# Performance work log

Measured on AMD Instinct MI355X. Metric: run time of the kernel, lower is better.

Reference implementation:

```python
import jax, jax.numpy as jnp
import numpy as np

L, B, E = 512, 4, 256
SCALE = 0.05  # keep sigmoid in a non-saturated range


def setup_inputs() -> dict:
    key = jax.random.key(0)
    ks = jax.random.split(key, 6)
    return {
        "emb": jax.random.normal(ks[0], (L, B, E), dtype=jnp.float32),
        "w1": jax.random.normal(ks[1], (E, E), dtype=jnp.float32) * SCALE,
        "w2": jax.random.normal(ks[2], (E, E), dtype=jnp.float32) * SCALE,
        "w3": jax.random.normal(ks[3], (E, E), dtype=jnp.float32) * SCALE,
        "b3": jax.random.normal(ks[4], (E,), dtype=jnp.float32) * SCALE,
        "w0": jax.random.normal(ks[5], (E,), dtype=jnp.float32) * SCALE,
    }


def reference(emb, w1, w2, w3, b3, w0):
    # emb: (L, B, E). torch Linear computes x @ W.T (+ b).
    Lq = emb.shape[0]
    u = jnp.einsum('lbe,fe->lbf', emb, w1)                      # w1(x_i), per key i
    q = jnp.einsum('lbe,fe->lbf', emb, w2)                      # w2(x_t), per query t
    c = jnp.einsum('lbe,fe->lbf', jnp.cumsum(emb, axis=0), w3) + b3  # w3(cumsum up to t)
    # gate[t, i, b, e] = sigmoid(u[i] + q[t] + c[t]); additive score via w0
    gate = jax.nn.sigmoid(u[None, :, :, :] + (q + c)[:, None, :, :])  # (L, L, B, E)
    scores = jnp.einsum('tibe,e->tib', gate, w0)                # (L, L, B)
    causal = jnp.tril(jnp.ones((Lq, Lq), dtype=emb.dtype))      # i <= t
    scores = scores * causal[:, :, None]
    # m_a[t] = sum_{i<=t} a_i * x_i
    return jnp.einsum('tib,ibe->tbe', scores, emb)              # (L, B, E)
```

## Files before the change

### kernel.cpp

```cpp
#include <hip/hip_runtime.h>
#include <hip/hip_bf16.h>

#define L_  512
#define B_  4
#define E_  256
#define TT  16
#define TI  64

typedef unsigned short u16;
#define NLOG2E (-1.44269504f)

__device__ __forceinline__ float bflo(unsigned u) { return __uint_as_float(u << 16); }
__device__ __forceinline__ float bfhi(unsigned u) { return __uint_as_float(u & 0xffff0000u); }

__device__ __forceinline__ unsigned pack_bf2(float x, float y) {
  __hip_bfloat162 h = __float22bfloat162_rn(make_float2(x, y));
  return *reinterpret_cast<unsigned*>(&h);
}

__device__ __forceinline__ float sigs(float xs) {
  float e = __builtin_amdgcn_exp2f(xs);
  return __builtin_amdgcn_rcpf(1.0f + e);
}

__global__ __launch_bounds__(256) void prescan_k(
    const float* __restrict__ emb, float* __restrict__ CE, float* __restrict__ out0) {
  const int bc = blockIdx.x;
  const int cg = threadIdx.x & 1;
  const int rk = threadIdx.x >> 1;
  const int col = bc * 8 + cg * 4;
  __shared__ float4 s_p[128][2];
  float4 part = {0.f, 0.f, 0.f, 0.f};
  for (int l = rk * 4; l < rk * 4 + 4; ++l) {
    float4 v = *(const float4*)(emb + (size_t)l * 1024 + col);
    part.x += v.x; part.y += v.y; part.z += v.z; part.w += v.w;
  }
  s_p[rk][cg] = part;
  __syncthreads();
  float4 run = {0.f, 0.f, 0.f, 0.f};
  for (int k = 0; k < rk; ++k) {
    float4 p = s_p[k][cg];
    run.x += p.x; run.y += p.y; run.z += p.z; run.w += p.w;
  }
  for (int l = rk * 4; l < rk * 4 + 4; ++l) {
    size_t o = (size_t)l * 1024 + col;
    float4 v = *(const float4*)(emb + o);
    run.x += v.x; run.y += v.y; run.z += v.z; run.w += v.w;
    *(float4*)(CE + o) = run;
  }
  const float4 z = {0.f, 0.f, 0.f, 0.f};
  float* op = out0 + ((size_t)bc * 256 + threadIdx.x) * 16;
#pragma unroll
  for (int j = 0; j < 4; ++j) *(float4*)(op + j * 4) = z;
}

__global__ __launch_bounds__(256) void gemm2_k(
    const float* __restrict__ emb, const float* __restrict__ CE,
    const float* __restrict__ w1, const float* __restrict__ w2, const float* __restrict__ w3,
    const float* __restrict__ b3, float* __restrict__ U, float* __restrict__ QC) {
  __shared__ float As[64 * 32], Ws[64 * 32];
  const int tid = threadIdx.x, tx = tid & 15, ty = tid >> 4;
  const int z = blockIdx.x;
  const bool isU = z < 128;
  const int y = isU ? z : z - 128;
  const int r0 = (y >> 2) * 64, f0 = (y & 3) * 64;
  const int nk = isU ? 8 : 16;
  float acc[4][4] = {};
  for (int kb = 0; kb < nk; ++kb) {
    const float* A = isU ? emb : (kb < 8 ? emb : CE);
    const float* W = isU ? w1 : (kb < 8 ? w2 : w3);
    const int kk = (kb & 7) * 32;
    for (int j = 0; j < 2; ++j) {
      int idx = j * 256 + tid;
      int r = idx >> 3, g = idx & 7;
      int gs = g ^ ((r >> 2) & 7);
      *(float4*)(As + r * 32 + gs * 4) = *(const float4*)(A + (size_t)(r0 + r) * E_ + kk + g * 4);
      *(float4*)(Ws + r * 32 + gs * 4) = *(const float4*)(W + (size_t)(f0 + r) * E_ + kk + g * 4);
    }
    __syncthreads();
#pragma unroll
    for (int g = 0; g < 8; ++g) {
      float4 a[4], w[4];
#pragma unroll
      for (int i = 0; i < 4; ++i) {
        int r = ty * 4 + i;
        a[i] = *(const float4*)(As + r * 32 + (g ^ ((r >> 2) & 7)) * 4);
        int f = tx * 4 + i;
        w[i] = *(const float4*)(Ws + f * 32 + (g ^ ((f >> 2) & 7)) * 4);
      }
#pragma unroll
      for (int i = 0; i < 4; ++i)
#pragma unroll
        for (int j = 0; j < 4; ++j)
          acc[i][j] += a[i].x * w[j].x + a[i].y * w[j].y + a[i].z * w[j].z + a[i].w * w[j].w;
    }
    __syncthreads();
  }
  if (isU) {
#pragma unroll
    for (int i = 0; i < 4; ++i) {
      float4 v = make_float4(acc[i][0] * NLOG2E, acc[i][1] * NLOG2E,
                             acc[i][2] * NLOG2E, acc[i][3] * NLOG2E);
      *(float4*)(U + (size_t)(r0 + ty * 4 + i) * E_ + f0 + tx * 4) = v;
    }
  } else {
    float4 bb = *(const float4*)(b3 + f0 + tx * 4);
#pragma unroll
    for (int i = 0; i < 4; ++i) {
      float4 v = make_float4(NLOG2E * (acc[i][0] + bb.x), NLOG2E * (acc[i][1] + bb.y),
                             NLOG2E * (acc[i][2] + bb.z), NLOG2E * (acc[i][3] + bb.w));
      *(float4*)(QC + (size_t)(r0 + ty * 4 + i) * E_ + f0 + tx * 4) = v;
    }
  }
}

__global__ __launch_bounds__(512, 8) void attn_main_k(
    const float* __restrict__ emb, const float* __restrict__ U,
    const float* __restrict__ QC, const float* __restrict__ w0g,
    float* __restrict__ out) {
  const int t0 = blockIdx.x * TT, i0 = blockIdx.y * TI, b = blockIdx.z;
  if (i0 > t0) return;

  __shared__ u16 tile[TI * 264];
  __shared__ float s_s[TT][TI];
  const int tid = threadIdx.x, wave = tid >> 6, lane = tid & 63;

  {
    const float* src = U + ((size_t)i0 * B_ + b) * E_ + lane * 4;
#pragma unroll
    for (int c = 0; c < 8; ++c) {
      int r = c * 8 + wave;
      float4 v = *(const float4*)(src + (size_t)r * (B_ * E_));
      *(uint2*)(tile + r * 264 + lane * 4) =
          make_uint2(pack_bf2(v.x, v.y), pack_bf2(v.z, v.w));
    }
  }
  __syncthreads();

  const int tA = t0 + wave * 2, tB = tA + 1;
  {
    int rA = __builtin_amdgcn_readfirstlane(tA * B_ + b);
    int rB = __builtin_amdgcn_readfirstlane(tB * B_ + b);
    const float* qA = QC + (size_t)rA * E_;
    const float* qB = QC + (size_t)rB * E_;
    const u16* urow = tile + lane * 264;
    float a0 = 0.f, a1 = 0.f, a2 = 0.f, a3 = 0.f;
    float c0 = 0.f, c1 = 0.f, c2 = 0.f, c3 = 0.f;
#pragma unroll 4
    for (int g = 0; g < 32; ++g) {
      uint4 raw = *(const uint4*)(urow + g * 8);
      float4 z0 = *(const float4*)(w0g + g * 8);
      float4 z1 = *(const float4*)(w0g + g * 8 + 4);
      float4 qa0 = *(const float4*)(qA + g * 8);
      float4 qa1 = *(const float4*)(qA + g * 8 + 4);
      float4 qb0 = *(const float4*)(qB + g * 8);
      float4 qb1 = *(const float4*)(qB + g * 8 + 4);
      float u0 = bflo(raw.x), u1 = bfhi(raw.x), u2 = bflo(raw.y), u3 = bfhi(raw.y);
      float u4 = bflo(raw.z), u5 = bfhi(raw.z), u6 = bflo(raw.w), u7 = bfhi(raw.w);
      a0 += z0.x * sigs(u0 + qa0.x); a1 += z0.y * sigs(u1 + qa0.y);
      a2 += z0.z * sigs(u2 + qa0.z); a3 += z0.w * sigs(u3 + qa0.w);
      a0 += z1.x * sigs(u4 + qa1.x); a1 += z1.y * sigs(u5 + qa1.y);
      a2 += z1.z * sigs(u6 + qa1.z); a3 += z1.w * sigs(u7 + qa1.w);
      c0 += z0.x * sigs(u0 + qb0.x); c1 += z0.y * sigs(u1 + qb0.y);
      c2 += z0.z * sigs(u2 + qb0.z); c3 += z0.w * sigs(u3 + qb0.w);
      c0 += z1.x * sigs(u4 + qb1.x); c1 += z1.y * sigs(u5 + qb1.y);
      c2 += z1.z * sigs(u6 + qb1.z); c3 += z1.w * sigs(u7 + qb1.w);
    }
    float sA = (a0 + a1) + (a2 + a3), sB = (c0 + c1) + (c2 + c3);
    int i = i0 + lane;
    s_s[wave * 2][lane]     = (i <= tA) ? sA : 0.f;
    s_s[wave * 2 + 1][lane] = (i <= tB) ? sB : 0.f;
  }
  __syncthreads();

  {
    const float* embp = emb + ((size_t)i0 * B_ + b) * E_ + lane * 4;
    const float* sAv = s_s[wave * 2];
    const float* sBv = s_s[wave * 2 + 1];
    int nI = min(TI, tB - i0 + 1);
    nI = (nI + 3) & ~3;
    float4 o0 = {0.f, 0.f, 0.f, 0.f}, o1 = {0.f, 0.f, 0.f, 0.f};
    for (int i = 0; i < nI; i += 4) {
#pragma unroll
      for (int k2 = 0; k2 < 4; ++k2) {
        float4 r = *(const float4*)(embp + (size_t)(i + k2) * (B_ * E_));
        float sa = sAv[i + k2], sb = sBv[i + k2];
        o0.x += sa * r.x; o0.y += sa * r.y; o0.z += sa * r.z; o0.w += sa * r.w;
        o1.x += sb * r.x; o1.y += sb * r.y; o1.z += sb * r.z; o1.w += sb * r.w;
      }
    }
    float* opA = out + ((size_t)tA * B_ + b) * E_ + lane * 4;
    float* opB = out + ((size_t)tB * B_ + b) * E_ + lane * 4;
    atomicAdd(opA + 0, o0.x); atomicAdd(opA + 1, o0.y);
    atomicAdd(opA + 2, o0.z); atomicAdd(opA + 3, o0.w);
    atomicAdd(opB + 0, o1.x); atomicAdd(opB + 1, o1.y);
    atomicAdd(opB + 2, o1.z); atomicAdd(opB + 3, o1.w);
  }
}

extern "C" void kernel_launch(void* const* d_in, const int* in_sizes, int n_in,
                              void* d_out, int out_size, void* d_ws, size_t ws_size,
                              hipStream_t stream) {
  const float* emb = (const float*)d_in[0];
  const float* w1  = (const float*)d_in[1];
  const float* w2  = (const float*)d_in[2];
  const float* w3  = (const float*)d_in[3];
  const float* b3  = (const float*)d_in[4];
  const float* w0  = (const float*)d_in[5];
  float* out = (float*)d_out;

  float* CE = (float*)d_ws;
  float* U  = CE + 524288;
  float* QC = U + 524288;

  prescan_k<<<dim3(128), 256, 0, stream>>>(emb, CE, out);
  gemm2_k<<<dim3(256), 256, 0, stream>>>(emb, CE, w1, w2, w3, b3, U, QC);
  attn_main_k<<<dim3(L_ / TT, L_ / TI, B_), 512, 0, stream>>>(emb, U, QC, w0, out);
}
```

Before: 173.1 us.

## Fuse GEMMs, scan and attention into one cooperative persistent kernel

Replaces the three-launch pipeline with a single cooperative kernel that runs the projection GEMMs, a cumsum applied after the w3 projection (using linearity so the scan runs on projected values), and the attention tiles in phases separated by grid syncs. The attention phase walks only the causal lower-triangle tiles through a persistent loop instead of launching and early-exiting masked blocks. This aims to remove launch overhead and idle blocks, at the cost of grid-sync latency and a per-call occupancy query on the host. A fallback path with a smaller-tile attention kernel is kept if the cooperative launch fails.

```diff
diff --git a/kernel.cpp b/kernel.cpp
--- a/kernel.cpp
+++ b/kernel.cpp
@@ -1,11 +1,12 @@
 #include <hip/hip_runtime.h>
 #include <hip/hip_bf16.h>
+#include <hip/hip_cooperative_groups.h>
+
+namespace cg = cooperative_groups;
 
 #define L_  512
 #define B_  4
 #define E_  256
-#define TT  16
-#define TI  64
 
 typedef unsigned short u16;
 #define NLOG2E (-1.44269504f)
@@ -21,6 +22,210 @@
 __device__ __forceinline__ float sigs(float xs) {
   float e = __builtin_amdgcn_exp2f(xs);
   return __builtin_amdgcn_rcpf(1.0f + e);
+}
+
+__global__ __launch_bounds__(512, 2) void coop_k(
+    const float* __restrict__ emb,
+    const float* __restrict__ w1, const float* __restrict__ w2, const float* __restrict__ w3,
+    const float* __restrict__ b3, const float* __restrict__ w0g,
+    float* __restrict__ U, float* __restrict__ Q2, float* __restrict__ V3,
+    float* __restrict__ out) {
+  __shared__ union {
+    struct { float As[2048], Wa[2048], Wb[2048]; } g;
+    float4 sp[64][8];
+    struct { u16 tile[64 * 264]; float ss[16][64]; } a;
+  } sm;
+
+  cg::grid_group grid = cg::this_grid();
+  const int tid = threadIdx.x, bid = blockIdx.x, nblk = gridDim.x;
+
+  for (int z = bid; z < 256; z += nblk) {
+    const bool isU = z < 128;
+    const int y = z & 127;
+    const int r0 = (y >> 2) * 64, f0 = (y & 3) * 64;
+    const int tx = tid & 15, ty = tid >> 4;
+    float acc0[2][4] = {}, acc1[2][4] = {};
+    for (int kb = 0; kb < 8; ++kb) {
+      const int kk = kb * 32;
+      {
+        int r = tid >> 3, g = tid & 7;
+        int gs = g ^ ((r >> 2) & 7);
+        *(float4*)(sm.g.As + r * 32 + gs * 4) =
+            *(const float4*)(emb + (size_t)(r0 + r) * E_ + kk + g * 4);
+        const float* Wp = isU ? w1 : w2;
+        *(float4*)(sm.g.Wa + r * 32 + gs * 4) =
+            *(const float4*)(Wp + (size_t)(f0 + r) * E_ + kk + g * 4);
+        if (!isU)
+          *(float4*)(sm.g.Wb + r * 32 + gs * 4) =
+              *(const float4*)(w3 + (size_t)(f0 + r) * E_ + kk + g * 4);
+      }
+      __syncthreads();
+#pragma unroll
+      for (int g = 0; g < 8; ++g) {
+        float4 a[2], wa[4], wb[4];
+#pragma unroll
+        for (int i = 0; i < 2; ++i) {
+          int r = ty * 2 + i;
+          a[i] = *(const float4*)(sm.g.As + r * 32 + (g ^ ((r >> 2) & 7)) * 4);
+        }
+#pragma unroll
+        for (int j = 0; j < 4; ++j) {
+          int f = tx * 4 + j;
+          int off = f * 32 + (g ^ ((f >> 2) & 7)) * 4;
+          wa[j] = *(const float4*)(sm.g.Wa + off);
+          if (!isU) wb[j] = *(const float4*)(sm.g.Wb + off);
+        }
+#pragma unroll
+        for (int i = 0; i < 2; ++i)
+#pragma unroll
+          for (int j = 0; j < 4; ++j) {
+            acc0[i][j] += a[i].x * wa[j].x + a[i].y * wa[j].y + a[i].z * wa[j].z + a[i].w * wa[j].w;
+            if (!isU)
+              acc1[i][j] += a[i].x * wb[j].x + a[i].y * wb[j].y + a[i].z * wb[j].z + a[i].w * wb[j].w;
+          }
+      }
+      __syncthreads();
+    }
+    if (isU) {
+#pragma unroll
+      for (int i = 0; i < 2; ++i) {
+        float4 v = make_float4(acc0[i][0] * NLOG2E, acc0[i][1] * NLOG2E,
+                               acc0[i][2] * NLOG2E, acc0[i][3] * NLOG2E);
+        *(float4*)(U + (size_t)(r0 + ty * 2 + i) * E_ + f0 + tx * 4) = v;
+      }
+    } else {
+#pragma unroll
+      for (int i = 0; i < 2; ++i) {
+        size_t o = (size_t)(r0 + ty * 2 + i) * E_ + f0 + tx * 4;
+        *(float4*)(Q2 + o) = make_float4(acc0[i][0], acc0[i][1], acc0[i][2], acc0[i][3]);
+        *(float4*)(V3 + o) = make_float4(acc1[i][0], acc1[i][1], acc1[i][2], acc1[i][3]);
+      }
+    }
+  }
+  for (int z = bid; z < 256; z += nblk) {
+    const float4 z4 = {0.f, 0.f, 0.f, 0.f};
+    *(float4*)(out + (size_t)z * 2048 + tid * 4) = z4;
+  }
+
+  grid.sync();
+
+  for (int sb = bid; sb < 32; sb += nblk) {
+    const int cgi = tid & 7, rk = tid >> 3;
+    const int c4 = sb * 8 + cgi;
+    const float* v3p = V3 + c4 * 4;
+    float4 part = {0.f, 0.f, 0.f, 0.f};
+    for (int l = rk * 8; l < rk * 8 + 8; ++l) {
+      float4 v = *(const float4*)(v3p + (size_t)l * 1024);
+      part.x += v.x; part.y += v.y; part.z += v.z; part.w += v.w;
+    }
+    sm.sp[rk][cgi] = part;
+    __syncthreads();
+    float4 run = {0.f, 0.f, 0.f, 0.f};
+    for (int k = 0; k < rk; ++k) {
+      float4 p = sm.sp[k][cgi];
+      run.x += p.x; run.y += p.y; run.z += p.z; run.w += p.w;
+    }
+    float4 bb = *(const float4*)(b3 + (c4 & 63) * 4);
+    float* q2p = Q2 + c4 * 4;
+    for (int l = rk * 8; l < rk * 8 + 8; ++l) {
+      size_t o = (size_t)l * 1024;
+      float4 v = *(const float4*)(v3p + o);
+      run.x += v.x; run.y += v.y; run.z += v.z; run.w += v.w;
+      float4 q = *(const float4*)(q2p + o);
+      float4 r;
+      r.x = NLOG2E * (q.x + bb.x + run.x);
+      r.y = NLOG2E * (q.y + bb.y + run.y);
+      r.z = NLOG2E * (q.z + bb.z + run.z);
+      r.w = NLOG2E * (q.w + bb.w + run.w);
+      *(float4*)(q2p + o) = r;
+    }
+    __syncthreads();
+  }
+
+  grid.sync();
+
+  const int wave = tid >> 6, lane = tid & 63;
+  for (int tile = bid; tile < 576; tile += nblk) {
+    const int b = tile & 3;
+    int j = tile >> 2;
+    int tt = 0;
+    while (true) { int c = (tt >> 2) + 1; if (j < c) break; j -= c; ++tt; }
+    const int t0 = tt * 16, i0 = j * 64;
+
+    __syncthreads();
+
+    {
+      const float* src = U + ((size_t)i0 * B_ + b) * E_ + lane * 4;
+#pragma unroll
+      for (int c = 0; c < 8; ++c) {
+        int r = c * 8 + wave;
+        float4 v = *(const float4*)(src + (size_t)r * (B_ * E_));
+        *(uint2*)(sm.a.tile + r * 264 + lane * 4) =
+            make_uint2(pack_bf2(v.x, v.y), pack_bf2(v.z, v.w));
+      }
+    }
+    __syncthreads();
+
+    const int tA = t0 + wave * 2, tB = tA + 1;
+    {
+      int rA = __builtin_amdgcn_readfirstlane(tA * B_ + b);
+      int rB = __builtin_amdgcn_readfirstlane(tB * B_ + b);
+      const float* qA = Q2 + (size_t)rA * E_;
+      const float* qB = Q2 + (size_t)rB * E_;
+      const u16* urow = sm.a.tile + lane * 264;
+      float a0 = 0.f, a1 = 0.f, a2 = 0.f, a3 = 0.f;
+      float c0 = 0.f, c1 = 0.f, c2 = 0.f, c3 = 0.f;
+#pragma unroll 4
+      for (int g = 0; g < 32; ++g) {
+        uint4 raw = *(const uint4*)(urow + g * 8);
+        float4 z0 = *(const float4*)(w0g + g * 8);
+        float4 z1 = *(const float4*)(w0g + g * 8 + 4);
+        float4 qa0 = *(const float4*)(qA + g * 8);
+        float4 qa1 = *(const float4*)(qA + g * 8 + 4);
+        float4 qb0 = *(const float4*)(qB + g * 8);
+        float4 qb1 = *(const float4*)(qB + g * 8 + 4);
+        float u0 = bflo(raw.x), u1 = bfhi(raw.x), u2 = bflo(raw.y), u3 = bfhi(raw.y);
+        float u4 = bflo(raw.z), u5 = bfhi(raw.z), u6 = bflo(raw.w), u7 = bfhi(raw.w);
+        a0 += z0.x * sigs(u0 + qa0.x); a1 += z0.y * sigs(u1 + qa0.y);
+        a2 += z0.z * sigs(u2 + qa0.z); a3 += z0.w * sigs(u3 + qa0.w);
+        a0 += z1.x * sigs(u4 + qa1.x); a1 += z1.y * sigs(u5 + qa1.y);
+        a2 += z1.z * sigs(u6 + qa1.z); a3 += z1.w * sigs(u7 + qa1.w);
+        c0 += z0.x * sigs(u0 + qb0.x); c1 += z0.y * sigs(u1 + qb0.y);
+        c2 += z0.z * sigs(u2 + qb0.z); c3 += z0.w * sigs(u3 + qb0.w);
+        c0 += z1.x * sigs(u4 + qb1.x); c1 += z1.y * sigs(u5 + qb1.y);
+        c2 += z1.z * sigs(u6 + qb1.z); c3 += z1.w * sigs(u7 + qb1.w);
+      }
+      float sA = (a0 + a1) + (a2 + a3), sB = (c0 + c1) + (c2 + c3);
+      int i = i0 + lane;
+      sm.a.ss[wave * 2][lane]     = (i <= tA) ? sA : 0.f;
+      sm.a.ss[wave * 2 + 1][lane] = (i <= tB) ? sB : 0.f;
+    }
+    __syncthreads();
+
+    {
+      const float* embp = emb + ((size_t)i0 * B_ + b) * E_ + lane * 4;
+      const float* sAv = sm.a.ss[wave * 2];
+      const float* sBv = sm.a.ss[wave * 2 + 1];
+      int nI = min(64, tB - i0 + 1);
+      nI = (nI + 3) & ~3;
+      float4 o0 = {0.f, 0.f, 0.f, 0.f}, o1 = {0.f, 0.f, 0.f, 0.f};
+      for (int i = 0; i < nI; i += 4) {
+#pragma unroll
+        for (int k2 = 0; k2 < 4; ++k2) {
+          float4 r = *(const float4*)(embp + (size_t)(i + k2) * (B_ * E_));
+          float sa = sAv[i + k2], sb = sBv[i + k2];
+          o0.x += sa * r.x; o0.y += sa * r.y; o0.z += sa * r.z; o0.w += sa * r.w;
+          o1.x += sb * r.x; o1.y += sb * r.y; o1.z += sb * r.z; o1.w += sb * r.w;
+        }
+      }
+      float* opA = out + ((size_t)tA * B_ + b) * E_ + lane * 4;
+      float* opB = out + ((size_t)tB * B_ + b) * E_ + lane * 4;
+      atomicAdd(opA + 0, o0.x); atomicAdd(opA + 1, o0.y);
+      atomicAdd(opA + 2, o0.z); atomicAdd(opA + 3, o0.w);
+      atomicAdd(opB + 0, o1.x); atomicAdd(opB + 1, o1.y);
+      atomicAdd(opB + 2, o1.z); atomicAdd(opB + 3, o1.w);
+    }
+  }
 }
 
 __global__ __launch_bounds__(256) void prescan_k(
@@ -114,22 +319,22 @@
   }
 }
 
-__global__ __launch_bounds__(512, 8) void attn_main_k(
+__global__ __launch_bounds__(256) void attn3_k(
     const float* __restrict__ emb, const float* __restrict__ U,
     const float* __restrict__ QC, const float* __restrict__ w0g,
     float* __restrict__ out) {
-  const int t0 = blockIdx.x * TT, i0 = blockIdx.y * TI, b = blockIdx.z;
+  const int t0 = blockIdx.x * 8, i0 = blockIdx.y * 64, b = blockIdx.z;
   if (i0 > t0) return;
 
-  __shared__ u16 tile[TI * 264];
-  __shared__ float s_s[TT][TI];
+  __shared__ u16 tile[64 * 264];
+  __shared__ float s_s[8][64];
   const int tid = threadIdx.x, wave = tid >> 6, lane = tid & 63;
 
   {
     const float* src = U + ((size_t)i0 * B_ + b) * E_ + lane * 4;
 #pragma unroll
-    for (int c = 0; c < 8; ++c) {
-      int r = c * 8 + wave;
+    for (int c = 0; c < 16; ++c) {
+      int r = c * 4 + wave;
       float4 v = *(const float4*)(src + (size_t)r * (B_ * E_));
       *(uint2*)(tile + r * 264 + lane * 4) =
           make_uint2(pack_bf2(v.x, v.y), pack_bf2(v.z, v.w));
@@ -177,7 +382,7 @@
     const float* embp = emb + ((size_t)i0 * B_ + b) * E_ + lane * 4;
     const float* sAv = s_s[wave * 2];
     const float* sBv = s_s[wave * 2 + 1];
-    int nI = min(TI, tB - i0 + 1);
+    int nI = min(64, tB - i0 + 1);
     nI = (nI + 3) & ~3;
     float4 o0 = {0.f, 0.f, 0.f, 0.f}, o1 = {0.f, 0.f, 0.f, 0.f};
     for (int i = 0; i < nI; i += 4) {
@@ -209,11 +414,26 @@
   const float* w0  = (const float*)d_in[5];
   float* out = (float*)d_out;
 
-  float* CE = (float*)d_ws;
-  float* U  = CE + 524288;
-  float* QC = U + 524288;
-
-  prescan_k<<<dim3(128), 256, 0, stream>>>(emb, CE, out);
-  gemm2_k<<<dim3(256), 256, 0, stream>>>(emb, CE, w1, w2, w3, b3, U, QC);
-  attn_main_k<<<dim3(L_ / TT, L_ / TI, B_), 512, 0, stream>>>(emb, U, QC, w0, out);
-}
+  float* buf0 = (float*)d_ws;
+  float* buf1 = buf0 + 524288;
+  float* buf2 = buf1 + 524288;
+
+  int maxB = 0;
+  hipError_t qe = hipOccupancyMaxActiveBlocksPerMultiprocessor(
+      &maxB, (const void*)coop_k, 512, 0);
+  if (qe == hipSuccess && maxB >= 1) {
+    int g = maxB * 256;
+    if (g > 512) g = 512;
+    void* args[] = {(void*)&emb, (void*)&w1, (void*)&w2, (void*)&w3,
+                    (void*)&b3, (void*)&w0, (void*)&buf0, (void*)&buf1,
+                    (void*)&buf2, (void*)&out};
+    hipError_t e = hipLaunchCooperativeKernel((const void*)coop_k, dim3(g),
+                                              dim3(512), args, 0, stream);
+    if (e == hipSuccess) return;
+    (void)hipGetLastError();
+  }
+
+  prescan_k<<<dim3(128), 256, 0, stream>>>(emb, buf0, out);
+  gemm2_k<<<dim3(256), 256, 0, stream>>>(emb, buf0, w1, w2, w3, b3, buf1, buf2);
+  attn3_k<<<dim3(64, 8, 4), 256, 0, stream>>>(emb, buf1, buf2, w0, out);
+}
```

New measurement: 157.2 us. 9.2% less time.
